# Optimization experiments

Hardware: AMD Instinct MI355X
Metric: run time of the kernel (lower is better)

## Reference

```python
import jax, jax.numpy as jnp
import numpy as np

EPS = 1e-12  # matches F.normalize default eps


def l2norm(x):
    n = jnp.sqrt(jnp.sum(x * x, axis=-1, keepdims=True))
    return x / jnp.maximum(n, EPS)


def setup_inputs() -> dict:
    key = jax.random.key(0)
    ks = jax.random.split(key, 14)
    B, Q, T, V = 128, 128, 64, 196
    Dv, Dt, E = 768, 768, 512
    s = 0.02  # kaiming-ish scale
    inp = {
        "visual_cls": jax.random.normal(ks[0], (Q, Dv), jnp.float32),
        "textual_cls": jax.random.normal(ks[1], (B, Dt), jnp.float32),
        "visual_tokens": jax.random.normal(ks[2], (Q, V, Dv), jnp.float32),
        "textual_tokens": jax.random.normal(ks[3], (B, T, Dt), jnp.float32),
        # linear params (torch nn.Linear convention: y = x @ W.T + b)
        "Wv_cls": jax.random.normal(ks[4], (E, Dv), jnp.float32) * s,
        "bv_cls": jnp.zeros((E,), jnp.float32),
        "Wt_cls": jax.random.normal(ks[5], (E, Dt), jnp.float32) * s,
        "bt_cls": jnp.zeros((E,), jnp.float32),
        "Wv_tok": jax.random.normal(ks[6], (E, Dv), jnp.float32) * s,
        "bv_tok": jnp.zeros((E,), jnp.float32),
        "Wt_tok": jax.random.normal(ks[7], (E, Dt), jnp.float32) * s,
        "bt_tok": jnp.zeros((E,), jnp.float32),
        "text_length": jax.random.randint(ks[8], (B,), 1, T + 1, jnp.int64),
    }
    return inp


def reference(visual_cls, textual_cls, visual_tokens, textual_tokens,
              Wv_cls, bv_cls, Wt_cls, bt_cls,
              Wv_tok, bv_tok, Wt_tok, bt_tok, text_length):
    # cls projections
    visual_embed_cls = visual_cls @ Wv_cls.T + bv_cls      # [Q, E]
    textual_embed_cls = textual_cls @ Wt_cls.T + bt_cls    # [B, E]
    # token projections + l2 norm
    ve = l2norm(visual_tokens @ Wv_tok.T + bv_tok)          # [Q, V, E]
    te = l2norm(textual_tokens @ Wt_tok.T + bt_tok)         # [B, T, E]

    B, T, _ = te.shape
    # text mask (built but NOT used in sim, faithful to original)
    text_mask = (jnp.arange(T)[None, :] < text_length[:, None]).astype(jnp.float32)

    # ColBERT-style MaxSim: [B, Q, T, V]
    logits = jnp.einsum('btd,qvd->bqtv', te, ve)
    Vdim = logits.shape[-1]
    Tdim = logits.shape[-2]
    t2v = jnp.sum(jnp.max(logits, axis=-1), axis=2) / Vdim  # [B, Q]
    v2t = jnp.sum(jnp.max(logits, axis=-2), axis=2) / Tdim  # [B, Q]
    text_to_image_sim = 0.5 * (t2v + v2t)                    # [B, Q]

    return (visual_embed_cls, textual_embed_cls, ve, te, text_mask,
            text_to_image_sim)
```

## Files before the change

kernel.cpp:

```cpp
#include <hip/hip_runtime.h>
#include <hip/hip_bf16.h>

typedef __bf16 bf16_t;
typedef __bf16 bf16x8 __attribute__((ext_vector_type(8)));
typedef __bf16 bf16x4 __attribute__((ext_vector_type(4)));
typedef float f32x4 __attribute__((ext_vector_type(4)));
typedef float f32x16 __attribute__((ext_vector_type(16)));

#define MFMA16(a, b, c) __builtin_amdgcn_mfma_f32_16x16x32_bf16((a), (b), (c), 0, 0, 0)
#define MFMA32(a, b, c) __builtin_amdgcn_mfma_f32_32x32x16_bf16((a), (b), (c), 0, 0, 0)

#define WN 393216
#define VP_ELEMS 14680064ULL
#define TP_ELEMS 4194304ULL

__device__ inline bf16x8 cvt8(const float* __restrict__ p) {
    f32x4 a = *reinterpret_cast<const f32x4*>(p);
    f32x4 b = *reinterpret_cast<const f32x4*>(p + 4);
    bf16x8 r;
    r[0] = (bf16_t)a[0]; r[1] = (bf16_t)a[1]; r[2] = (bf16_t)a[2]; r[3] = (bf16_t)a[3];
    r[4] = (bf16_t)b[0]; r[5] = (bf16_t)b[1]; r[6] = (bf16_t)b[2]; r[7] = (bf16_t)b[3];
    return r;
}

__device__ __forceinline__ void gload_lds16(const bf16_t* g, bf16_t* l) {
    __builtin_amdgcn_global_load_lds(
        (const __attribute__((address_space(1))) void*)g,
        (__attribute__((address_space(3))) void*)l, 16, 0, 0);
}

__global__ __launch_bounds__(256) void cvt_w4(
    const float* __restrict__ s0, const float* __restrict__ s1,
    const float* __restrict__ s2, const float* __restrict__ s3,
    bf16_t* __restrict__ d)
{
    int i = blockIdx.x * 256 + threadIdx.x;
    int seg = i / (WN / 4);
    int off = i - seg * (WN / 4);
    const float* s = (seg == 0) ? s0 : (seg == 1) ? s1 : (seg == 2) ? s2 : s3;
    f32x4 v = reinterpret_cast<const f32x4*>(s)[off];
    bf16x4 r;
    r[0] = (bf16_t)v[0]; r[1] = (bf16_t)v[1];
    r[2] = (bf16_t)v[2]; r[3] = (bf16_t)v[3];
    reinterpret_cast<bf16x4*>(d)[i] = r;
}

__global__ __launch_bounds__(256) void zero_tail(bf16_t* __restrict__ vp)
{
    int i = blockIdx.x * 256 + threadIdx.x;
    int off = (i & 63) * 8;
    int ks  = (i >> 6) & 3;
    int c   = (i >> 8) & 7;
    int q   = i >> 11;
    size_t addr = ((size_t)q * 224 + c * 28 + 24 + ks) * 512 + off;
    *reinterpret_cast<f32x4*>(vp + addr) = (f32x4){0.f, 0.f, 0.f, 0.f};
}

template<int PACKED>
__global__ __launch_bounds__(256) void proj_all(
    const float* __restrict__ vtok, const float* __restrict__ ttok,
    const float* __restrict__ vcls, const float* __restrict__ tcls,
    const bf16_t* __restrict__ w_all,
    const float* __restrict__ bvc, const float* __restrict__ btc,
    const float* __restrict__ bvt, const float* __restrict__ btt,
    float* __restrict__ out_base,
    bf16_t* __restrict__ bve, bf16_t* __restrict__ bte)
{
    const int tid  = threadIdx.x;
    const int wave = tid >> 6;
    const int lane = tid & 63;
    const int l16  = lane & 15;
    const int quad = lane >> 4;
    const int e0   = wave * 128;
    const int id   = blockIdx.x;

    const float* A; const bf16_t* W; const float* bias;
    float* out; bf16_t* outb; int seg, m0;
    if (id < 784)       { seg = 0; A = vtok; W = w_all + 2 * WN; bias = bvt;
                          out = out_base + 131072;   outb = bve; m0 = id * 32; }
    else if (id < 1040) { seg = 1; A = ttok; W = w_all + 3 * WN; bias = btt;
                          out = out_base + 12976128; outb = bte; m0 = (id - 784) * 32; }
    else if (id < 1044) { seg = 2; A = vcls; W = w_all;          bias = bvc;
                          out = out_base;             outb = nullptr; m0 = (id - 1040) * 32; }
    else                { seg = 3; A = tcls; W = w_all + WN;     bias = btc;
                          out = out_base + 65536;     outb = nullptr; m0 = (id - 1044) * 32; }

    f32x4 acc[2][8];
#pragma unroll
    for (int rt = 0; rt < 2; ++rt)
#pragma unroll
        for (int t = 0; t < 8; ++t) acc[rt][t] = (f32x4){0.f, 0.f, 0.f, 0.f};

    const float* ar0 = A + (size_t)(m0 + l16) * 768 + quad * 8;
    const float* ar1 = ar0 + (size_t)16 * 768;

    for (int k0 = 0; k0 < 768; k0 += 32) {
        bf16x8 a0 = cvt8(ar0 + k0);
        bf16x8 a1 = cvt8(ar1 + k0);
#pragma unroll
        for (int t = 0; t < 8; ++t) {
            bf16x8 wv = *reinterpret_cast<const bf16x8*>(
                W + (size_t)(e0 + t * 16 + l16) * 768 + quad * 8 + k0);
            acc[0][t] = MFMA16(a0, wv, acc[0][t]);
            acc[1][t] = MFMA16(a1, wv, acc[1][t]);
        }
    }

#pragma unroll
    for (int t = 0; t < 8; ++t) {
        float bv = bias[e0 + t * 16 + l16];
#pragma unroll
        for (int rt = 0; rt < 2; ++rt)
#pragma unroll
            for (int r = 0; r < 4; ++r) acc[rt][t][r] += bv;
    }

    float inv[2][4];
#pragma unroll
    for (int rt = 0; rt < 2; ++rt)
#pragma unroll
        for (int r = 0; r < 4; ++r) inv[rt][r] = 1.f;

    __shared__ float sq[4][32];
    if (seg <= 1) {
#pragma unroll
        for (int rt = 0; rt < 2; ++rt)
#pragma unroll
            for (int r = 0; r < 4; ++r) {
                float s = 0.f;
#pragma unroll
                for (int t = 0; t < 8; ++t) s += acc[rt][t][r] * acc[rt][t][r];
                s += __shfl_xor(s, 1);
                s += __shfl_xor(s, 2);
                s += __shfl_xor(s, 4);
                s += __shfl_xor(s, 8);
                if (l16 == 0) sq[wave][rt * 16 + quad * 4 + r] = s;
            }
        __syncthreads();
#pragma unroll
        for (int rt = 0; rt < 2; ++rt)
#pragma unroll
            for (int r = 0; r < 4; ++r) {
                int row = rt * 16 + quad * 4 + r;
                float tot = sq[0][row] + sq[1][row] + sq[2][row] + sq[3][row];
                inv[rt][r] = 1.0f / fmaxf(sqrtf(tot), 1e-12f);
            }
    }

#pragma unroll
    for (int rt = 0; rt < 2; ++rt)
#pragma unroll
        for (int r = 0; r < 4; ++r) {
            const int   R  = m0 + rt * 16 + quad * 4 + r;
            const float is = inv[rt][r];
            const size_t lin = (size_t)R * 512 + e0 + l16;
#pragma unroll
            for (int t = 0; t < 8; ++t)
                out[lin + t * 16] = acc[rt][t][r] * is;

            if (seg <= 1) {
                if (!PACKED) {
#pragma unroll
                    for (int t = 0; t < 8; ++t)
                        outb[lin + t * 16] = (bf16_t)(acc[rt][t][r] * is);
                } else {
                    size_t fb0; int elem, stride_c;
                    if (seg == 0) {
                        int qq = R / 196, vv = R - qq * 196;
                        fb0  = (size_t)qq * 224 + (vv >> 5) * 4;
                        elem = (((l16 >> 3) * 32 + (vv & 31)) << 3) | (l16 & 7);
                        stride_c = 28;
                    } else {
                        int bb = R >> 6;
                        fb0  = (size_t)bb * 64 + ((R >> 5) & 1) * 4;
                        elem = (((l16 >> 3) * 32 + (R & 31)) << 3) | (l16 & 7);
                        stride_c = 8;
                    }
#pragma unroll
                    for (int t = 0; t < 8; ++t) {
                        int c  = wave * 2 + (t >> 2);
                        int ks = t & 3;
                        outb[(fb0 + (size_t)c * stride_c + ks) * 512 + elem] =
                            (bf16_t)(acc[rt][t][r] * is);
                    }
                }
            }
        }
}

__global__ __launch_bounds__(512, 4) void maxsim32p(
    const bf16_t* __restrict__ tp,
    const bf16_t* __restrict__ vp,
    float* __restrict__ sim)
{
    const int tid  = threadIdx.x;
    const int wave = tid >> 6;
    const int lane = tid & 63;
    const int l32  = lane & 31;
    const int h    = lane >> 5;
    const int vh   = wave >> 2;
    const int bhat = (wave >> 1) & 1;
    const int tt   = wave & 1;
    const int vt0  = vh * 4;

    const int n  = blockIdx.x;
    const int q  = n >> 6;
    const int bp = n & 63;
    const int b  = bp * 2 + bhat;

    __shared__ bf16_t vs[2][14336];
    float* red = (float*)(void*)&vs[0][0];

    f32x16 acc[4];
#pragma unroll
    for (int j = 0; j < 4; ++j)
#pragma unroll
        for (int r = 0; r < 16; ++r) acc[j][r] = 0.f;

    const bf16_t* vq = vp + (size_t)q * 114688;
    const bf16_t* tb = tp + (size_t)b * 32768;

    auto issue = [&](int buf, int c) {
#pragma unroll
        for (int g = 0; g < 4; ++g) {
            int f = wave + g * 8;
            if (f < 28)
                gload_lds16(vq + (size_t)c * 14336 + f * 512 + lane * 8,
                            &vs[buf][f * 512]);
        }
    };

    issue(0, 0);
#pragma unroll
    for (int c = 0; c < 8; ++c) {
        __syncthreads();
        if (c < 7) issue((c + 1) & 1, c + 1);
        bf16x8 a[4];
        const bf16_t* ta = tb + (size_t)(c * 8 + tt * 4) * 512 + lane * 8;
#pragma unroll
        for (int ks = 0; ks < 4; ++ks)
            a[ks] = *reinterpret_cast<const bf16x8*>(ta + ks * 512);
        const bf16_t* bbase = &vs[c & 1][vt0 * 2048 + lane * 8];
#pragma unroll
        for (int ks = 0; ks < 4; ++ks) {
#pragma unroll
            for (int j = 0; j < 3; ++j) {
                bf16x8 bv = *reinterpret_cast<const bf16x8*>(
                    bbase + (j * 4 + ks) * 512);
                acc[j] = MFMA32(a[ks], bv, acc[j]);
            }
            if (vh == 0) {
                bf16x8 bv = *reinterpret_cast<const bf16x8*>(
                    bbase + (12 + ks) * 512);
                acc[3] = MFMA32(a[ks], bv, acc[3]);
            }
        }
    }

#pragma unroll
    for (int reg = 0; reg < 16; ++reg) {
        float m = fmaxf(acc[0][reg], acc[1][reg]);
        if (vh == 0) {
            m = fmaxf(m, acc[2][reg]);
            m = fmaxf(m, acc[3][reg]);
        } else if (l32 < 4) {
            m = fmaxf(m, acc[2][reg]);
        }
        m = fmaxf(m, __shfl_xor(m, 1));
        m = fmaxf(m, __shfl_xor(m, 2));
        m = fmaxf(m, __shfl_xor(m, 4));
        m = fmaxf(m, __shfl_xor(m, 8));
        m = fmaxf(m, __shfl_xor(m, 16));
        if (l32 == 0) {
            int row = tt * 32 + (reg & 3) + 8 * (reg >> 2) + 4 * h;
            red[(bhat * 2 + vh) * 64 + row] = m;
        }
    }
#pragma unroll
    for (int j = 0; j < 3; ++j) {
        float m = acc[j][0];
#pragma unroll
        for (int reg = 1; reg < 16; ++reg) m = fmaxf(m, acc[j][reg]);
        m = fmaxf(m, __shfl_xor(m, 32));
        if (h == 0) red[256 + (bhat * 2 + tt) * 224 + (vt0 + j) * 32 + l32] = m;
    }
    if (vh == 0) {
        float m = acc[3][0];
#pragma unroll
        for (int reg = 1; reg < 16; ++reg) m = fmaxf(m, acc[3][reg]);
        m = fmaxf(m, __shfl_xor(m, 32));
        if (h == 0) red[256 + (bhat * 2 + tt) * 224 + 3 * 32 + l32] = m;
    }
    __syncthreads();

    if (wave == 0) {
#pragma unroll
        for (int bi = 0; bi < 2; ++bi) {
            float t = fmaxf(red[(bi * 2 + 0) * 64 + lane],
                            red[(bi * 2 + 1) * 64 + lane]);
            float cc = 0.f;
            for (int v = lane; v < 196; v += 64)
                cc += fmaxf(red[256 + (bi * 2 + 0) * 224 + v],
                            red[256 + (bi * 2 + 1) * 224 + v]);
#pragma unroll
            for (int mk = 1; mk <= 32; mk <<= 1) {
                t  += __shfl_xor(t, mk);
                cc += __shfl_xor(cc, mk);
            }
            if (lane == 0)
                sim[(size_t)(bp * 2 + bi) * 128 + q] =
                    0.5f * (t * (1.0f / 196.0f) + cc * (1.0f / 64.0f));
        }
    }
}

__global__ __launch_bounds__(256) void maxsim32(
    const bf16_t* __restrict__ te,
    const bf16_t* __restrict__ ve,
    float* __restrict__ sim)
{
    const int tid  = threadIdx.x;
    const int wave = tid >> 6;
    const int lane = tid & 63;
    const int l32  = lane & 31;
    const int h    = lane >> 5;
    const int bhat = wave >> 1;
    const int tt   = wave & 1;

    const int n  = blockIdx.x;
    const int q  = n >> 6;
    const int bp = n & 63;
    const int b  = bp * 2 + bhat;

    __shared__ bf16_t vs[2][224 * 64];
    __shared__ float  tmax_s[2][64];
    __shared__ float  vmax_s[2][2][224];

    f32x16 acc[7];
#pragma unroll
    for (int vt = 0; vt < 7; ++vt)
#pragma unroll
        for (int r = 0; r < 16; ++r) acc[vt][r] = 0.f;

    auto issue = [&](int buf, int c) {
        for (int g = wave; g < 28; g += 4) {
            int r   = g * 8 + (lane >> 3);
            int sr  = r < 196 ? r : 195;
            int seg = (lane & 7) ^ (lane >> 3);
            gload_lds16(ve + ((size_t)q * 196 + sr) * 512 + c * 64 + seg * 8,
                        &vs[buf][g * 512]);
        }
    };

    const size_t tbase = ((size_t)b * 64 + tt * 32 + l32) * 512;

    issue(0, 0);
#pragma unroll
    for (int c = 0; c < 8; ++c) {
        __syncthreads();
        if (c < 7) issue((c + 1) & 1, c + 1);
        bf16x8 a[4];
#pragma unroll
        for (int ks = 0; ks < 4; ++ks)
            a[ks] = *reinterpret_cast<const bf16x8*>(
                te + tbase + c * 64 + ks * 16 + h * 8);
        const int buf = c & 1;
#pragma unroll
        for (int ks = 0; ks < 4; ++ks)
#pragma unroll
            for (int vt = 0; vt < 7; ++vt) {
                int row  = vt * 32 + l32;
                int phys = (ks * 2 + h) ^ (row & 7);
                bf16x8 bv = *reinterpret_cast<const bf16x8*>(
                    &vs[buf][row * 64 + phys * 8]);
                acc[vt] = MFMA32(a[ks], bv, acc[vt]);
            }
    }

#pragma unroll
    for (int reg = 0; reg < 16; ++reg) {
        float m = acc[0][reg];
#pragma unroll
        for (int vt = 1; vt < 6; ++vt) m = fmaxf(m, acc[vt][reg]);
        if (l32 < 4) m = fmaxf(m, acc[6][reg]);
        m = fmaxf(m, __shfl_xor(m, 1));
        m = fmaxf(m, __shfl_xor(m, 2));
        m = fmaxf(m, __shfl_xor(m, 4));
        m = fmaxf(m, __shfl_xor(m, 8));
        m = fmaxf(m, __shfl_xor(m, 16));
        if (l32 == 0) {
            int row = tt * 32 + (reg & 3) + 8 * (reg >> 2) + 4 * h;
            tmax_s[bhat][row] = m;
        }
    }
#pragma unroll
    for (int vt = 0; vt < 7; ++vt) {
        float m = acc[vt][0];
#pragma unroll
        for (int reg = 1; reg < 16; ++reg) m = fmaxf(m, acc[vt][reg]);
        m = fmaxf(m, __shfl_xor(m, 32));
        if (h == 0) vmax_s[bhat][tt][vt * 32 + l32] = m;
    }
    __syncthreads();

    if (wave == 0) {
        float t0 = tmax_s[0][lane];
        float t1 = tmax_s[1][lane];
        float c0 = 0.f, c1 = 0.f;
        for (int v = lane; v < 196; v += 64) {
            c0 += fmaxf(vmax_s[0][0][v], vmax_s[0][1][v]);
            c1 += fmaxf(vmax_s[1][0][v], vmax_s[1][1][v]);
        }
#pragma unroll
        for (int mk = 1; mk <= 32; mk <<= 1) {
            t0 += __shfl_xor(t0, mk);
            t1 += __shfl_xor(t1, mk);
            c0 += __shfl_xor(c0, mk);
            c1 += __shfl_xor(c1, mk);
        }
        if (lane == 0) {
            sim[(size_t)(bp * 2 + 0) * 128 + q] = 0.5f * (t0 * (1.0f / 196.0f) + c0 * (1.0f / 64.0f));
            sim[(size_t)(bp * 2 + 1) * 128 + q] = 0.5f * (t1 * (1.0f / 196.0f) + c1 * (1.0f / 64.0f));
        }
    }
}

__global__ __launch_bounds__(256) void proj_fb(
    const float* __restrict__ A, const float* __restrict__ Wf,
    const float* __restrict__ bias, float* __restrict__ out, int do_l2)
{
    const int tid  = threadIdx.x;
    const int wave = tid >> 6;
    const int lane = tid & 63;
    const int l16  = lane & 15;
    const int quad = lane >> 4;
    const int m0   = blockIdx.x * 16;
    const int e0   = wave * 128;

    f32x4 acc[8];
#pragma unroll
    for (int t = 0; t < 8; ++t) acc[t] = (f32x4){0.f, 0.f, 0.f, 0.f};
    const float* arow = A + (size_t)(m0 + l16) * 768 + quad * 8;
    for (int k0 = 0; k0 < 768; k0 += 32) {
        bf16x8 af = cvt8(arow + k0);
#pragma unroll
        for (int t = 0; t < 8; ++t) {
            bf16x8 wv = cvt8(Wf + (size_t)(e0 + t * 16 + l16) * 768 + quad * 8 + k0);
            acc[t] = MFMA16(af, wv, acc[t]);
        }
    }
#pragma unroll
    for (int t = 0; t < 8; ++t) {
        float bv = bias[e0 + t * 16 + l16];
#pragma unroll
        for (int r = 0; r < 4; ++r) acc[t][r] += bv;
    }
    float inv[4] = {1.f, 1.f, 1.f, 1.f};
    __shared__ float sq[4][16];
    if (do_l2) {
#pragma unroll
        for (int r = 0; r < 4; ++r) {
            float s = 0.f;
#pragma unroll
            for (int t = 0; t < 8; ++t) s += acc[t][r] * acc[t][r];
            s += __shfl_xor(s, 1); s += __shfl_xor(s, 2);
            s += __shfl_xor(s, 4); s += __shfl_xor(s, 8);
            if (l16 == 0) sq[wave][quad * 4 + r] = s;
        }
        __syncthreads();
#pragma unroll
        for (int r = 0; r < 4; ++r) {
            float tot = sq[0][quad * 4 + r] + sq[1][quad * 4 + r]
                      + sq[2][quad * 4 + r] + sq[3][quad * 4 + r];
            inv[r] = 1.0f / fmaxf(sqrtf(tot), 1e-12f);
        }
    }
#pragma unroll
    for (int t = 0; t < 8; ++t)
#pragma unroll
        for (int r = 0; r < 4; ++r)
            out[(size_t)(m0 + quad * 4 + r) * 512 + (e0 + t * 16 + l16)] =
                acc[t][r] * inv[r];
}

__global__ __launch_bounds__(256) void maxsim_fb(
    const float* __restrict__ te, const float* __restrict__ ve,
    float* __restrict__ sim)
{
    const int tid  = threadIdx.x;
    const int wave = tid >> 6;
    const int lane = tid & 63;
    const int l16  = lane & 15;
    const int quad = lane >> 4;
    const int q    = blockIdx.x >> 6;
    const int bp   = blockIdx.x & 63;

    __shared__ bf16_t vsl[208 * 72];
    __shared__ float  maxt_s[2][4][208];
    __shared__ float  t2v_part[2][4];

    f32x4 acc0[13], acc1[13];
#pragma unroll
    for (int vt = 0; vt < 13; ++vt) {
        acc0[vt] = (f32x4){0.f, 0.f, 0.f, 0.f};
        acc1[vt] = (f32x4){0.f, 0.f, 0.f, 0.f};
    }
    const size_t toff0 = ((size_t)(bp * 2) * 64 + wave * 16 + l16) * 512 + quad * 8;
    const size_t toff1 = toff0 + (size_t)64 * 512;

    for (int k0 = 0; k0 < 512; k0 += 64) {
        __syncthreads();
        for (int s = tid; s < 416; s += 256) {
            const int row  = s >> 1;
            const int half = s & 1;
            const int vsrc = row < 196 ? row : 195;
            bf16x8 tmp[4];
            const size_t goff = ((size_t)q * 196 + vsrc) * 512 + k0 + half * 32;
#pragma unroll
            for (int j = 0; j < 4; ++j) tmp[j] = cvt8(ve + goff + j * 8);
            bf16_t* dst = &vsl[row * 72 + half * 32];
#pragma unroll
            for (int j = 0; j < 4; ++j)
                *reinterpret_cast<bf16x8*>(dst + j * 8) = tmp[j];
        }
        __syncthreads();
#pragma unroll
        for (int ks = 0; ks < 2; ++ks) {
            bf16x8 a0 = cvt8(te + toff0 + k0 + ks * 32);
            bf16x8 a1 = cvt8(te + toff1 + k0 + ks * 32);
#pragma unroll
            for (int vt = 0; vt < 13; ++vt) {
                bf16x8 bv = *reinterpret_cast<const bf16x8*>(
                    &vsl[(vt * 16 + l16) * 72 + ks * 32 + quad * 8]);
                acc0[vt] = MFMA16(a0, bv, acc0[vt]);
                acc1[vt] = MFMA16(a1, bv, acc1[vt]);
            }
        }
    }
#pragma unroll
    for (int bi = 0; bi < 2; ++bi) {
        const f32x4* acc = bi ? acc1 : acc0;
        float sum_maxv = 0.f;
#pragma unroll
        for (int r = 0; r < 4; ++r) {
            float m = -3.0e38f;
#pragma unroll
            for (int vt = 0; vt < 13; ++vt) {
                int v = vt * 16 + l16;
                if (v < 196) m = fmaxf(m, acc[vt][r]);
            }
            m = fmaxf(m, __shfl_xor(m, 1));
            m = fmaxf(m, __shfl_xor(m, 2));
            m = fmaxf(m, __shfl_xor(m, 4));
            m = fmaxf(m, __shfl_xor(m, 8));
            sum_maxv += m;
        }
        sum_maxv += __shfl_xor(sum_maxv, 16);
        sum_maxv += __shfl_xor(sum_maxv, 32);
        if (lane == 0) t2v_part[bi][wave] = sum_maxv;
#pragma unroll
        for (int vt = 0; vt < 13; ++vt) {
            float m = fmaxf(fmaxf(acc[vt][0], acc[vt][1]),
                            fmaxf(acc[vt][2], acc[vt][3]));
            m = fmaxf(m, __shfl_xor(m, 16));
            m = fmaxf(m, __shfl_xor(m, 32));
            if (lane < 16) maxt_s[bi][wave][vt * 16 + l16] = m;
        }
    }
    __syncthreads();
    if (wave == 0) {
#pragma unroll
        for (int bi = 0; bi < 2; ++bi) {
            float s_row = t2v_part[bi][0] + t2v_part[bi][1]
                        + t2v_part[bi][2] + t2v_part[bi][3];
            float s_col = 0.f;
            for (int v = lane; v < 196; v += 64) {
                float m = fmaxf(fmaxf(maxt_s[bi][0][v], maxt_s[bi][1][v]),
                                fmaxf(maxt_s[bi][2][v], maxt_s[bi][3][v]));
                s_col += m;
            }
            s_col += __shfl_xor(s_col, 1);
            s_col += __shfl_xor(s_col, 2);
            s_col += __shfl_xor(s_col, 4);
            s_col += __shfl_xor(s_col, 8);
            s_col += __shfl_xor(s_col, 16);
            s_col += __shfl_xor(s_col, 32);
            if (lane == 0)
                sim[(size_t)(bp * 2 + bi) * 128 + q] =
                    0.5f * (s_row * (1.0f / 196.0f) + s_col * (1.0f / 64.0f));
        }
    }
}

__global__ void mask_kernel(const int* __restrict__ len, float* __restrict__ mask)
{
    int i = blockIdx.x * 256 + threadIdx.x;
    int is64 = (len[1] == 0) ? 1 : 0;
    if (i < 128 * 64) {
        int b = i >> 6;
        int t = i & 63;
        int L = is64 ? len[2 * b] : len[b];
        mask[i] = (t < L) ? 1.0f : 0.0f;
    }
}

extern "C" void kernel_launch(void* const* d_in, const int* in_sizes, int n_in,
                              void* d_out, int out_size, void* d_ws, size_t ws_size,
                              hipStream_t stream)
{
    int idx[13] = {0, 1, 2, 3, 4, 5, 6, 7, 8, 9, 10, 11, 12};
    if (in_sizes && n_in >= 13) {
        bool dict = (in_sizes[2] == 19267584) && (in_sizes[4] == 393216);
        if (!dict) {
            static const int alpha_sizes[13] = {393216, 393216, 393216, 393216,
                                                512, 512, 512, 512, 128,
                                                98304, 6291456, 98304, 19267584};
            bool alpha = true;
            for (int i = 0; i < 13; ++i)
                if (in_sizes[i] != alpha_sizes[i]) { alpha = false; break; }
            if (alpha) {
                const int m[13] = {11, 9, 12, 10, 2, 6, 0, 4, 3, 7, 1, 5, 8};
                for (int i = 0; i < 13; ++i) idx[i] = m[i];
            }
        }
    }

    const float* visual_cls     = (const float*)d_in[idx[0]];
    const float* textual_cls    = (const float*)d_in[idx[1]];
    const float* visual_tokens  = (const float*)d_in[idx[2]];
    const float* textual_tokens = (const float*)d_in[idx[3]];
    const float* Wv_cls = (const float*)d_in[idx[4]];
    const float* bv_cls = (const float*)d_in[idx[5]];
    const float* Wt_cls = (const float*)d_in[idx[6]];
    const float* bt_cls = (const float*)d_in[idx[7]];
    const float* Wv_tok = (const float*)d_in[idx[8]];
    const float* bv_tok = (const float*)d_in[idx[9]];
    const float* Wt_tok = (const float*)d_in[idx[10]];
    const float* bt_tok = (const float*)d_in[idx[11]];
    const int*   text_length = (const int*)d_in[idx[12]];

    float* out    = (float*)d_out;
    float* o_vcls = out;
    float* o_tcls = out + 65536;
    float* o_ve   = out + 131072;
    float* o_te   = out + 12976128;
    float* o_mask = out + 17170432;
    float* o_sim  = out + 17178624;

    const size_t NVE = 12845056;
    const size_t NTE = 4194304;
    const size_t need_new = (4 * (size_t)WN + VP_ELEMS + TP_ELEMS) * 2;
    const size_t need_old = (4 * (size_t)WN + NVE + NTE) * 2;

    dim3 blk(256);
    if (ws_size >= need_new) {
        bf16_t* w_all = (bf16_t*)d_ws;
        bf16_t* vp    = w_all + 4 * (size_t)WN;
        bf16_t* tp    = vp + VP_ELEMS;
        cvt_w4<<<(4 * WN / 4 + 255) / 256, blk, 0, stream>>>(Wv_cls, Wt_cls, Wv_tok, Wt_tok, w_all);
        zero_tail<<<1024, blk, 0, stream>>>(vp);
        proj_all<1><<<1048, blk, 0, stream>>>(visual_tokens, textual_tokens,
                                              visual_cls, textual_cls, w_all,
                                              bv_cls, bt_cls, bv_tok, bt_tok,
                                              out, vp, tp);
        mask_kernel<<<32, blk, 0, stream>>>(text_length, o_mask);
        maxsim32p<<<128 * 64, dim3(512), 0, stream>>>(tp, vp, o_sim);
    } else if (ws_size >= need_old) {
        bf16_t* w_all = (bf16_t*)d_ws;
        bf16_t* b_ve  = w_all + 4 * (size_t)WN;
        bf16_t* b_te  = b_ve + NVE;
        cvt_w4<<<(4 * WN / 4 + 255) / 256, blk, 0, stream>>>(Wv_cls, Wt_cls, Wv_tok, Wt_tok, w_all);
        proj_all<0><<<1048, blk, 0, stream>>>(visual_tokens, textual_tokens,
                                              visual_cls, textual_cls, w_all,
                                              bv_cls, bt_cls, bv_tok, bt_tok,
                                              out, b_ve, b_te);
        mask_kernel<<<32, blk, 0, stream>>>(text_length, o_mask);
        maxsim32<<<128 * 64, blk, 0, stream>>>(b_te, b_ve, o_sim);
    } else {
        proj_fb<<<8,    blk, 0, stream>>>(visual_cls,     Wv_cls, bv_cls, o_vcls, 0);
        proj_fb<<<8,    blk, 0, stream>>>(textual_cls,    Wt_cls, bt_cls, o_tcls, 0);
        proj_fb<<<1568, blk, 0, stream>>>(visual_tokens,  Wv_tok, bv_tok, o_ve, 1);
        proj_fb<<<512,  blk, 0, stream>>>(textual_tokens, Wt_tok, bt_tok, o_te, 1);
        mask_kernel<<<32, blk, 0, stream>>>(text_length, o_mask);
        maxsim_fb<<<128 * 64, blk, 0, stream>>>(o_te, o_ve, o_sim);
    }
}
```

Measured before the change: 611.7 us.

## Repartition maxsim waves so each LDS tile feeds two text batches

Each wave in the maxsim kernel now computes both text batches of its block against a two-column slice of visual tiles. Previously each wave handled one batch against up to four columns. Every B fragment read from LDS is now reused for two MFMAs, which halves LDS reads per MFMA, and the A-fragment global loads are software-pipelined one k-step ahead. Which waves take the short final slice alternates with block parity to balance load. In exchange, each wave issues more global loads for the text operand, and the reduction scratch layout grows.

```diff
diff --git a/kernel.cpp b/kernel.cpp
--- a/kernel.cpp
+++ b/kernel.cpp
@@ -198,27 +198,30 @@
     const int lane = tid & 63;
     const int l32  = lane & 31;
     const int h    = lane >> 5;
-    const int vh   = wave >> 2;
-    const int bhat = (wave >> 1) & 1;
     const int tt   = wave & 1;
-    const int vt0  = vh * 4;
 
     const int n  = blockIdx.x;
     const int q  = n >> 6;
     const int bp = n & 63;
-    const int b  = bp * 2 + bhat;
+
+    const int p   = ((wave >> 1) + 2 * (n & 1)) & 3;
+    const int vt0 = 2 * p;
 
     __shared__ bf16_t vs[2][14336];
     float* red = (float*)(void*)&vs[0][0];
 
-    f32x16 acc[4];
-#pragma unroll
-    for (int j = 0; j < 4; ++j)
-#pragma unroll
-        for (int r = 0; r < 16; ++r) acc[j][r] = 0.f;
-
-    const bf16_t* vq = vp + (size_t)q * 114688;
-    const bf16_t* tb = tp + (size_t)b * 32768;
+    f32x16 acc[2][2];
+#pragma unroll
+    for (int bi = 0; bi < 2; ++bi)
+#pragma unroll
+        for (int j = 0; j < 2; ++j)
+#pragma unroll
+            for (int r = 0; r < 16; ++r) acc[bi][j][r] = 0.f;
+
+    const bf16_t* vq  = vp + (size_t)q * 114688;
+    const bf16_t* tb0 = tp + (size_t)(bp * 2) * 32768
+                           + (size_t)(tt * 4) * 512 + lane * 8;
+    const bf16_t* tb1 = tb0 + 32768;
 
     auto issue = [&](int buf, int c) {
 #pragma unroll
@@ -235,73 +238,79 @@
     for (int c = 0; c < 8; ++c) {
         __syncthreads();
         if (c < 7) issue((c + 1) & 1, c + 1);
-        bf16x8 a[4];
-        const bf16_t* ta = tb + (size_t)(c * 8 + tt * 4) * 512 + lane * 8;
-#pragma unroll
-        for (int ks = 0; ks < 4; ++ks)
-            a[ks] = *reinterpret_cast<const bf16x8*>(ta + ks * 512);
-        const bf16_t* bbase = &vs[c & 1][vt0 * 2048 + lane * 8];
+
+        const size_t cb = (size_t)(c * 8) * 512;
+        bf16x8 a0[2], a1[2];
+        a0[0] = *reinterpret_cast<const bf16x8*>(tb0 + cb);
+        a1[0] = *reinterpret_cast<const bf16x8*>(tb1 + cb);
+
+        const bf16_t* bb = &vs[c & 1][lane * 8];
 #pragma unroll
         for (int ks = 0; ks < 4; ++ks) {
-#pragma unroll
-            for (int j = 0; j < 3; ++j) {
+            const int s = ks & 1;
+            if (ks < 3) {
+                a0[s ^ 1] = *reinterpret_cast<const bf16x8*>(tb0 + cb + (ks + 1) * 512);
+                a1[s ^ 1] = *reinterpret_cast<const bf16x8*>(tb1 + cb + (ks + 1) * 512);
+            }
+            {
                 bf16x8 bv = *reinterpret_cast<const bf16x8*>(
-                    bbase + (j * 4 + ks) * 512);
-                acc[j] = MFMA32(a[ks], bv, acc[j]);
-            }
-            if (vh == 0) {
+                    bb + (vt0 * 4 + ks) * 512);
+                acc[0][0] = MFMA32(a0[s], bv, acc[0][0]);
+                acc[1][0] = MFMA32(a1[s], bv, acc[1][0]);
+            }
+            if (p < 3) {
                 bf16x8 bv = *reinterpret_cast<const bf16x8*>(
-                    bbase + (12 + ks) * 512);
-                acc[3] = MFMA32(a[ks], bv, acc[3]);
+                    bb + ((vt0 + 1) * 4 + ks) * 512);
+                acc[0][1] = MFMA32(a0[s], bv, acc[0][1]);
+                acc[1][1] = MFMA32(a1[s], bv, acc[1][1]);
             }
         }
     }
 
 #pragma unroll
     for (int reg = 0; reg < 16; ++reg) {
-        float m = fmaxf(acc[0][reg], acc[1][reg]);
-        if (vh == 0) {
-            m = fmaxf(m, acc[2][reg]);
-            m = fmaxf(m, acc[3][reg]);
-        } else if (l32 < 4) {
-            m = fmaxf(m, acc[2][reg]);
-        }
-        m = fmaxf(m, __shfl_xor(m, 1));
-        m = fmaxf(m, __shfl_xor(m, 2));
-        m = fmaxf(m, __shfl_xor(m, 4));
-        m = fmaxf(m, __shfl_xor(m, 8));
-        m = fmaxf(m, __shfl_xor(m, 16));
-        if (l32 == 0) {
-            int row = tt * 32 + (reg & 3) + 8 * (reg >> 2) + 4 * h;
-            red[(bhat * 2 + vh) * 64 + row] = m;
-        }
-    }
-#pragma unroll
-    for (int j = 0; j < 3; ++j) {
-        float m = acc[j][0];
-#pragma unroll
-        for (int reg = 1; reg < 16; ++reg) m = fmaxf(m, acc[j][reg]);
-        m = fmaxf(m, __shfl_xor(m, 32));
-        if (h == 0) red[256 + (bhat * 2 + tt) * 224 + (vt0 + j) * 32 + l32] = m;
-    }
-    if (vh == 0) {
-        float m = acc[3][0];
-#pragma unroll
-        for (int reg = 1; reg < 16; ++reg) m = fmaxf(m, acc[3][reg]);
-        m = fmaxf(m, __shfl_xor(m, 32));
-        if (h == 0) red[256 + (bhat * 2 + tt) * 224 + 3 * 32 + l32] = m;
+#pragma unroll
+        for (int bi = 0; bi < 2; ++bi) {
+            float m;
+            if (p < 3) m = fmaxf(acc[bi][0][reg], acc[bi][1][reg]);
+            else       m = (l32 < 4) ? acc[bi][0][reg] : -3.0e38f;
+            m = fmaxf(m, __shfl_xor(m, 1));
+            m = fmaxf(m, __shfl_xor(m, 2));
+            m = fmaxf(m, __shfl_xor(m, 4));
+            m = fmaxf(m, __shfl_xor(m, 8));
+            m = fmaxf(m, __shfl_xor(m, 16));
+            if (l32 == 0) {
+                int row = tt * 32 + (reg & 3) + 8 * (reg >> 2) + 4 * h;
+                red[(bi * 4 + p) * 64 + row] = m;
+            }
+        }
+    }
+#pragma unroll
+    for (int j = 0; j < 2; ++j) {
+        if (j == 1 && p == 3) continue;
+#pragma unroll
+        for (int bi = 0; bi < 2; ++bi) {
+            float m = acc[bi][j][0];
+#pragma unroll
+            for (int reg = 1; reg < 16; ++reg) m = fmaxf(m, acc[bi][j][reg]);
+            m = fmaxf(m, __shfl_xor(m, 32));
+            if (h == 0)
+                red[512 + (bi * 2 + tt) * 224 + (vt0 + j) * 32 + l32] = m;
+        }
     }
     __syncthreads();
 
     if (wave == 0) {
 #pragma unroll
         for (int bi = 0; bi < 2; ++bi) {
-            float t = fmaxf(red[(bi * 2 + 0) * 64 + lane],
-                            red[(bi * 2 + 1) * 64 + lane]);
+            float t = red[(bi * 4 + 0) * 64 + lane];
+#pragma unroll
+            for (int pp = 1; pp < 4; ++pp)
+                t = fmaxf(t, red[(bi * 4 + pp) * 64 + lane]);
             float cc = 0.f;
             for (int v = lane; v < 196; v += 64)
-                cc += fmaxf(red[256 + (bi * 2 + 0) * 224 + v],
-                            red[256 + (bi * 2 + 1) * 224 + v]);
+                cc += fmaxf(red[512 + (bi * 2 + 0) * 224 + v],
+                            red[512 + (bi * 2 + 1) * 224 + v]);
 #pragma unroll
             for (int mk = 1; mk <= 32; mk <<= 1) {
                 t  += __shfl_xor(t, mk);
```

Result: slower. 666.4 us (+8.9%).

## Triple-buffer V tiles in half-size chunks with manual vmcnt waits

Applied to the files above, without the earlier changes.

Rebuilds the MaxSim kernel's main loop to stream visual tokens into LDS in 16 half-size chunks across three buffers instead of 8 chunks across two. Each step waits with an explicit s_waitcnt on vmcnt and then issues a raw barrier, so two loads can be in flight while the MFMAs run. Text-side A fragments are prefetched one chunk ahead into ping-pong registers. This trades more barriers, a hand-counted wait scheme, and a separate reduction buffer for better overlap of global-to-LDS loads with compute.

```diff
diff --git a/kernel.cpp b/kernel.cpp
--- a/kernel.cpp
+++ b/kernel.cpp
@@ -208,8 +208,8 @@
     const int bp = n & 63;
     const int b  = bp * 2 + bhat;
 
-    __shared__ bf16_t vs[2][14336];
-    float* red = (float*)(void*)&vs[0][0];
+    __shared__ bf16_t vs[3][7168];
+    __shared__ float  red[1152];
 
     f32x16 acc[4];
 #pragma unroll
@@ -218,44 +218,83 @@
         for (int r = 0; r < 16; ++r) acc[j][r] = 0.f;
 
     const bf16_t* vq = vp + (size_t)q * 114688;
-    const bf16_t* tb = tp + (size_t)b * 32768;
+    const bf16_t* tb = tp + (size_t)b * 32768 + lane * 8;
 
     auto issue = [&](int buf, int c) {
 #pragma unroll
-        for (int g = 0; g < 4; ++g) {
-            int f = wave + g * 8;
-            if (f < 28)
-                gload_lds16(vq + (size_t)c * 14336 + f * 512 + lane * 8,
-                            &vs[buf][f * 512]);
+        for (int g = 0; g < 2; ++g) {
+            int slot = wave + g * 8;
+            int s2   = (slot >= 14) ? (slot - 14) : slot;
+            int f    = (s2 >> 1) * 4 + (c & 1) * 2 + (s2 & 1);
+            gload_lds16(vq + (size_t)(c >> 1) * 14336 + (size_t)f * 512 + lane * 8,
+                        &vs[buf][s2 * 512]);
         }
     };
 
-    issue(0, 0);
-#pragma unroll
-    for (int c = 0; c < 8; ++c) {
-        __syncthreads();
-        if (c < 7) issue((c + 1) & 1, c + 1);
-        bf16x8 a[4];
-        const bf16_t* ta = tb + (size_t)(c * 8 + tt * 4) * 512 + lane * 8;
-#pragma unroll
-        for (int ks = 0; ks < 4; ++ks)
-            a[ks] = *reinterpret_cast<const bf16x8*>(ta + ks * 512);
-        const bf16_t* bbase = &vs[c & 1][vt0 * 2048 + lane * 8];
-#pragma unroll
-        for (int ks = 0; ks < 4; ++ks) {
-#pragma unroll
-            for (int j = 0; j < 3; ++j) {
-                bf16x8 bv = *reinterpret_cast<const bf16x8*>(
-                    bbase + (j * 4 + ks) * 512);
-                acc[j] = MFMA32(a[ks], bv, acc[j]);
-            }
-            if (vh == 0) {
-                bf16x8 bv = *reinterpret_cast<const bf16x8*>(
-                    bbase + (12 + ks) * 512);
-                acc[3] = MFMA32(a[ks], bv, acc[3]);
-            }
-        }
-    }
+    bf16x8 aA[2], aB[2];
+
+#define PIN asm volatile("" ::: "memory")
+
+    issue(0, 0); PIN;
+    issue(1, 1); PIN;
+    {
+        const size_t fo = (size_t)(tt * 4) * 512;
+        aA[0] = *reinterpret_cast<const bf16x8*>(tb + fo);
+        aA[1] = *reinterpret_cast<const bf16x8*>(tb + fo + 512);
+    }
+    PIN;
+
+#define CHUNK(c, NW)                                                         \
+    asm volatile("s_waitcnt vmcnt(" #NW ") lgkmcnt(0)" ::: "memory");        \
+    __builtin_amdgcn_s_barrier();                                            \
+    PIN;                                                                     \
+    if ((c) < 14) issue(((c) + 2) % 3, (c) + 2);                             \
+    PIN;                                                                     \
+    if ((c) < 15) {                                                          \
+        const size_t fo = (size_t)(((((c) + 1) >> 1) * 8) + tt * 4           \
+                                   + (((c) + 1) & 1) * 2) * 512;             \
+        bf16x8* an = ((c) & 1) ? aA : aB;                                    \
+        an[0] = *reinterpret_cast<const bf16x8*>(tb + fo);                   \
+        an[1] = *reinterpret_cast<const bf16x8*>(tb + fo + 512);             \
+    }                                                                        \
+    PIN;                                                                     \
+    {                                                                        \
+        const bf16_t* bb = &vs[(c) % 3][vt0 * 1024 + lane * 8];              \
+        bf16x8* ac = ((c) & 1) ? aB : aA;                                    \
+        _Pragma("unroll")                                                    \
+        for (int s = 0; s < 2; ++s) {                                        \
+            _Pragma("unroll")                                                \
+            for (int j = 0; j < 3; ++j) {                                    \
+                bf16x8 bv = *reinterpret_cast<const bf16x8*>(                \
+                    bb + (j * 2 + s) * 512);                                 \
+                acc[j] = MFMA32(ac[s], bv, acc[j]);                          \
+            }                                                                \
+            if (vh == 0) {                                                   \
+                bf16x8 bv = *reinterpret_cast<const bf16x8*>(                \
+                    bb + (6 + s) * 512);                                     \
+                acc[3] = MFMA32(ac[s], bv, acc[3]);                          \
+            }                                                                \
+        }                                                                    \
+    }
+
+    CHUNK(0, 4)
+    CHUNK(1, 6)
+    CHUNK(2, 6)
+    CHUNK(3, 6)
+    CHUNK(4, 6)
+    CHUNK(5, 6)
+    CHUNK(6, 6)
+    CHUNK(7, 6)
+    CHUNK(8, 6)
+    CHUNK(9, 6)
+    CHUNK(10, 6)
+    CHUNK(11, 6)
+    CHUNK(12, 6)
+    CHUNK(13, 6)
+    CHUNK(14, 6)
+    CHUNK(15, 4)
+#undef CHUNK
+#undef PIN
 
 #pragma unroll
     for (int reg = 0; reg < 16; ++reg) {
```

Result: slower. 625.8 us (+2.3%).

## Pre-swizzle weights into MFMA fragment order and stage A tile in LDS

Applied to the files above, without the earlier changes.

The weight-conversion kernel now writes bf16 weights in a fragment-major layout, so each wave's MFMA B-operand load is one contiguous 16-byte-per-lane read. The projection kernel converts the 32x768 fp32 activation tile into XOR-swizzled LDS once per block instead of reloading and converting it from global memory every k-step. It also adds a launch_bounds occupancy hint of two blocks. The cost is 48KB of LDS per block, which may limit residency, plus a more complex index mapping in the conversion kernel.

```diff
diff --git a/kernel.cpp b/kernel.cpp
--- a/kernel.cpp
+++ b/kernel.cpp
@@ -34,15 +34,18 @@
     const float* __restrict__ s2, const float* __restrict__ s3,
     bf16_t* __restrict__ d)
 {
-    int i = blockIdx.x * 256 + threadIdx.x;
-    int seg = i / (WN / 4);
-    int off = i - seg * (WN / 4);
+    int g = blockIdx.x * 256 + threadIdx.x;
+    int seg = g / 49152;
+    int rem = g - seg * 49152;
+    int frag = rem >> 6;
+    int lane = rem & 63;
+    int k  = frag % 24;
+    int et = frag / 24;
+    int row = et * 16 + (lane & 15);
+    int col = k * 32 + (lane >> 4) * 8;
     const float* s = (seg == 0) ? s0 : (seg == 1) ? s1 : (seg == 2) ? s2 : s3;
-    f32x4 v = reinterpret_cast<const f32x4*>(s)[off];
-    bf16x4 r;
-    r[0] = (bf16_t)v[0]; r[1] = (bf16_t)v[1];
-    r[2] = (bf16_t)v[2]; r[3] = (bf16_t)v[3];
-    reinterpret_cast<bf16x4*>(d)[i] = r;
+    bf16x8 r = cvt8(s + (size_t)row * 768 + col);
+    *reinterpret_cast<bf16x8*>(d + (size_t)g * 8) = r;
 }
 
 __global__ __launch_bounds__(256) void zero_tail(bf16_t* __restrict__ vp)
@@ -57,7 +60,7 @@
 }
 
 template<int PACKED>
-__global__ __launch_bounds__(256) void proj_all(
+__global__ __launch_bounds__(256, 2) void proj_all(
     const float* __restrict__ vtok, const float* __restrict__ ttok,
     const float* __restrict__ vcls, const float* __restrict__ tcls,
     const bf16_t* __restrict__ w_all,
@@ -85,22 +88,38 @@
     else                { seg = 3; A = tcls; W = w_all + WN;     bias = btc;
                           out = out_base + 65536;     outb = nullptr; m0 = (id - 1044) * 32; }
 
+    __shared__ bf16_t As[32 * 768];
+#pragma unroll
+    for (int it = 0; it < 12; ++it) {
+        int idx = it * 256 + tid;
+        int row = idx / 96;
+        int cg  = idx - row * 96;
+        bf16x8 v = cvt8(A + (size_t)(m0 + row) * 768 + cg * 8);
+        int byte = (row * 1536 + cg * 16) ^ ((row & 7) << 4);
+        *reinterpret_cast<bf16x8*>(reinterpret_cast<char*>(As) + byte) = v;
+    }
+    __syncthreads();
+
     f32x4 acc[2][8];
 #pragma unroll
     for (int rt = 0; rt < 2; ++rt)
 #pragma unroll
         for (int t = 0; t < 8; ++t) acc[rt][t] = (f32x4){0.f, 0.f, 0.f, 0.f};
 
-    const float* ar0 = A + (size_t)(m0 + l16) * 768 + quad * 8;
-    const float* ar1 = ar0 + (size_t)16 * 768;
-
-    for (int k0 = 0; k0 < 768; k0 += 32) {
-        bf16x8 a0 = cvt8(ar0 + k0);
-        bf16x8 a1 = cvt8(ar1 + k0);
+    const bf16_t* wb = W + (size_t)(wave * 8) * 24 * 512 + lane * 8;
+    const int axor = (l16 & 7) << 4;
+
+    for (int k = 0; k < 24; ++k) {
+        int b0 = ((l16)      * 1536 + (k * 4 + quad) * 16) ^ axor;
+        int b1 = ((l16 + 16) * 1536 + (k * 4 + quad) * 16) ^ axor;
+        bf16x8 a0 = *reinterpret_cast<const bf16x8*>(
+            reinterpret_cast<const char*>(As) + b0);
+        bf16x8 a1 = *reinterpret_cast<const bf16x8*>(
+            reinterpret_cast<const char*>(As) + b1);
 #pragma unroll
         for (int t = 0; t < 8; ++t) {
             bf16x8 wv = *reinterpret_cast<const bf16x8*>(
-                W + (size_t)(e0 + t * 16 + l16) * 768 + quad * 8 + k0);
+                wb + (size_t)(t * 24 + k) * 512);
             acc[0][t] = MFMA16(a0, wv, acc[0][t]);
             acc[1][t] = MFMA16(a1, wv, acc[1][t]);
         }
@@ -657,7 +676,7 @@
         bf16_t* w_all = (bf16_t*)d_ws;
         bf16_t* vp    = w_all + 4 * (size_t)WN;
         bf16_t* tp    = vp + VP_ELEMS;
-        cvt_w4<<<(4 * WN / 4 + 255) / 256, blk, 0, stream>>>(Wv_cls, Wt_cls, Wv_tok, Wt_tok, w_all);
+        cvt_w4<<<768, blk, 0, stream>>>(Wv_cls, Wt_cls, Wv_tok, Wt_tok, w_all);
         zero_tail<<<1024, blk, 0, stream>>>(vp);
         proj_all<1><<<1048, blk, 0, stream>>>(visual_tokens, textual_tokens,
                                               visual_cls, textual_cls, w_all,
@@ -669,7 +688,7 @@
         bf16_t* w_all = (bf16_t*)d_ws;
         bf16_t* b_ve  = w_all + 4 * (size_t)WN;
         bf16_t* b_te  = b_ve + NVE;
-        cvt_w4<<<(4 * WN / 4 + 255) / 256, blk, 0, stream>>>(Wv_cls, Wt_cls, Wv_tok, Wt_tok, w_all);
+        cvt_w4<<<768, blk, 0, stream>>>(Wv_cls, Wt_cls, Wv_tok, Wt_tok, w_all);
         proj_all<0><<<1048, blk, 0, stream>>>(visual_tokens, textual_tokens,
                                               visual_cls, textual_cls, w_all,
                                               bv_cls, bt_cls, bv_tok, bt_tok,
```

After: 507.0 us. -17.1%, faster.
